# Kernel optimization log

Measured on AMD Instinct MI355X. Metric: run time of the kernel, lower is better.

The kernel has to match this reference:

```python
import jax, jax.numpy as jnp
import numpy as np

NEG_INF = -9e15  # matches torch's -9000000000000000.0 mask value
ALPHA = 0.2      # LeakyReLU negative slope


def setup_inputs() -> dict:
    key = jax.random.key(0)
    k1, k2, k3, k4 = jax.random.split(key, 4)
    B, N, Fin, Fout, H = 32, 512, 256, 64, 8
    x = jax.random.normal(k1, (B, N, Fin), dtype=jnp.float32)
    adj = (jax.random.uniform(k2, (B, N, N)) < 0.5).astype(jnp.float32)
    # W: Linear(in_features, out_features*n_heads, bias=False) weight, stored as (Fin, Fout*H)
    W = jax.random.normal(k3, (Fin, Fout * H), dtype=jnp.float32) / np.sqrt(Fin).astype(np.float32)
    # a: attention vector per head over concat(src,dst) features -> (H, 2*Fout)
    a = jax.random.normal(k4, (H, 2 * Fout), dtype=jnp.float32) * 0.1
    return {"x": x, "adj": adj, "W": W, "a": a}


def reference(x, adj, W, a):
    # x: (B,N,Fin), adj: (B,N,N), W: (Fin, H*F), a: (H, 2F)
    B, N, _ = x.shape
    H, twoF = a.shape
    F = twoF // 2
    h = (x @ W).reshape(B, N, H, F)  # (B,N,H,F)
    # Decompose concat-score: e_ij = lrelu(h_i . a_src + h_j . a_dst) -- same math
    # as (cat(h_i,h_j) * a).sum(-1) without materializing (B,N,N,H,2F).
    s_src = jnp.einsum('bnhf,hf->bnh', h, a[:, :F])  # (B,N,H)
    s_dst = jnp.einsum('bnhf,hf->bnh', h, a[:, F:])  # (B,N,H)
    e = s_src[:, :, None, :] + s_dst[:, None, :, :]  # (B,N,N,H)
    e = jax.nn.leaky_relu(e, negative_slope=ALPHA)
    e = jnp.where(adj[..., None] > 0, e, NEG_INF)
    attn = jax.nn.softmax(e, axis=2)  # softmax over neighbors j (dim=2)
    # dropout omitted (eval mode / p effectively 0 for the reference baseline)
    h_prime = jnp.einsum('bijh,bjhf->bihf', attn, h)  # (B,N,H,F)
    return h_prime.reshape(B, N, H * F)  # concat=True
```

## Files before the change

kernel.cpp:

```cpp
#include <hip/hip_runtime.h>
#include <hip/hip_bf16.h>
#include <stdint.h>


#define ALPHA  0.2f
#define ESCALE 1.4426950408889634f

typedef __bf16 bf16x8 __attribute__((ext_vector_type(8)));
typedef __bf16 bf16x4 __attribute__((ext_vector_type(4)));
typedef float  f32x4  __attribute__((ext_vector_type(4)));

#if __has_builtin(__builtin_amdgcn_exp2f)
#define EXP2(x) __builtin_amdgcn_exp2f(x)
#else
#define EXP2(x) exp2f(x)
#endif

#define HT_STRIDE 520
#define WT_STRIDE 264

__device__ inline bf16x8 ld8(const float* p) {
    float4 a0 = *(const float4*)p;
    float4 a1 = *(const float4*)(p + 4);
    bf16x8 r;
    r[0]=(__bf16)a0.x; r[1]=(__bf16)a0.y; r[2]=(__bf16)a0.z; r[3]=(__bf16)a0.w;
    r[4]=(__bf16)a1.x; r[5]=(__bf16)a1.y; r[6]=(__bf16)a1.z; r[7]=(__bf16)a1.w;
    return r;
}

__global__ __launch_bounds__(512) void k0_all(const float* __restrict__ x,
                                              const float* __restrict__ W,
                                              const float* __restrict__ adj,
                                              __bf16* __restrict__ xbf,
                                              __bf16* __restrict__ Wbf,
                                              unsigned* __restrict__ mask) {
    __shared__ float tile[64][65];
    const int blk = blockIdx.x, tid = threadIdx.x;
    if (blk < 1024) {
        long c = (long)blk * 512 + tid;
        int s  = (int)(c & 7);
        int r  = (int)((c >> 3) & 511);
        int kc = (int)((c >> 12) & 3);
        int b  = (int)(c >> 14);
        const float* src = x + (((long)b * 512 + r) * 256 + kc * 64 + s * 8);
        float4 a0 = *(const float4*)src;
        float4 a1 = *(const float4*)(src + 4);
        bf16x8 o;
        o[0]=(__bf16)a0.x; o[1]=(__bf16)a0.y; o[2]=(__bf16)a0.z; o[3]=(__bf16)a0.w;
        o[4]=(__bf16)a1.x; o[5]=(__bf16)a1.y; o[6]=(__bf16)a1.z; o[7]=(__bf16)a1.w;
        *(bf16x8*)(xbf + c * 8) = o;
    } else if (blk < 1056) {
        int bi = blk - 1024;
        int kt = bi & 3, ft = bi >> 2;
        int ff = tid & 63;
        #pragma unroll
        for (int i = 0; i < 8; ++i) {
            int kk = (tid >> 6) + i * 8;
            tile[kk][ff] = W[(long)(kt * 64 + kk) * 512 + ft * 64 + ff];
        }
        __syncthreads();
        int kk2 = tid & 63;
        #pragma unroll
        for (int i = 0; i < 8; ++i) {
            int ff2 = (tid >> 6) + i * 8;
            Wbf[(long)(ft * 64 + ff2) * 256 + kt * 64 + kk2] = (__bf16)tile[kk2][ff2];
        }
    } else {
        const int T2 = (blk - 1056) * 512 + tid;
        const int w    = T2 & 3;
        const int quad = (T2 >> 2) & 3;
        const int row  = (T2 >> 4) & 511;
        const int b    = T2 >> 13;
        const float* p = adj + ((long)b * 512 + row) * 512 + quad * 8;
        unsigned word = 0;
        #pragma unroll
        for (int k = 0; k < 4; ++k) {
            const float* qp = p + (w * 4 + k) * 32;
            float4 a0 = *(const float4*)qp;
            float4 a1 = *(const float4*)(qp + 4);
            unsigned byte =  (a0.x > 0.f ? 1u : 0u)
                          | ((a0.y > 0.f ? 1u : 0u) << 1)
                          | ((a0.z > 0.f ? 1u : 0u) << 2)
                          | ((a0.w > 0.f ? 1u : 0u) << 3)
                          | ((a1.x > 0.f ? 1u : 0u) << 4)
                          | ((a1.y > 0.f ? 1u : 0u) << 5)
                          | ((a1.z > 0.f ? 1u : 0u) << 6)
                          | ((a1.w > 0.f ? 1u : 0u) << 7);
            word |= byte << (8 * k);
        }
        mask[T2] = word;
    }
}

struct SmemK1 {
    __bf16 Wt[64 * 256];
    __bf16 Xt[256 * 64];
    float  asrc[64], adst[64];
};

__global__ __launch_bounds__(512, 4) void k1_gemm(const __bf16* __restrict__ xbf,
                                                  const __bf16* __restrict__ Wbf,
                                                  const float* __restrict__ a,
                                                  __bf16* __restrict__ hT,
                                                  float* __restrict__ ssrc,
                                                  float* __restrict__ sdst) {
    __shared__ SmemK1 sm;
    const int b = blockIdx.x, h = blockIdx.y, zz = blockIdx.z;
    const int tid  = threadIdx.x;
    const int wave = tid >> 6, lane = tid & 63;
    const int quad = lane >> 4, col = lane & 15;
    const int row0 = zz * 256;

    if (tid < 128) {
        float v = a[h * 128 + tid] * ESCALE;
        if (tid < 64) sm.asrc[tid] = v; else sm.adst[tid - 64] = v;
    }
    {
        const uint4* src = (const uint4*)(Wbf + (long)h * 64 * 256);
        #pragma unroll
        for (int i = 0; i < 4; ++i) {
            int c = tid + i * 512;
            int f = c >> 5, s = c & 31;
            int sw = (s & 24) | ((s & 7) ^ (f & 7));
            *(uint4*)((char*)sm.Wt + f * 512 + sw * 16) = src[c];
        }
    }
    {
        const uint4* src = (const uint4*)(xbf + (((long)b * 4 + 0) * 512 + row0) * 64);
        #pragma unroll
        for (int i = 0; i < 4; ++i) {
            int c = tid + i * 512;
            int r = c >> 3, s = c & 7;
            *(uint4*)((char*)sm.Xt + r * 128 + ((s ^ (r & 7)) * 16)) = src[c];
        }
    }
    __syncthreads();

    f32x4 acc[2][4] = {};
    #pragma unroll
    for (int kc = 0; kc < 4; ++kc) {
        #pragma unroll
        for (int sk = 0; sk < 2; ++sk) {
            bf16x8 av[2], bv[4];
            #pragma unroll
            for (int it = 0; it < 2; ++it) {
                int r = wave * 32 + it * 16 + col;
                int g = (sk * 4 + quad) ^ (r & 7);
                av[it] = *(const bf16x8*)((const char*)sm.Xt + r * 128 + g * 16);
            }
            #pragma unroll
            for (int nt = 0; nt < 4; ++nt) {
                int n = nt * 16 + col;
                int G = kc * 8 + sk * 4 + quad;
                int Gs = (G & 24) | ((G & 7) ^ (n & 7));
                bv[nt] = *(const bf16x8*)((const char*)sm.Wt + n * 512 + Gs * 16);
            }
            #pragma unroll
            for (int it = 0; it < 2; ++it)
                #pragma unroll
                for (int nt = 0; nt < 4; ++nt)
                    acc[it][nt] = __builtin_amdgcn_mfma_f32_16x16x32_bf16(av[it], bv[nt], acc[it][nt], 0, 0, 0);
        }
        if (kc < 3) {
            __syncthreads();
            const uint4* src = (const uint4*)(xbf + (((long)b * 4 + kc + 1) * 512 + row0) * 64);
            #pragma unroll
            for (int i = 0; i < 4; ++i) {
                int c = tid + i * 512;
                int r = c >> 3, s = c & 7;
                *(uint4*)((char*)sm.Xt + r * 128 + ((s ^ (r & 7)) * 16)) = src[c];
            }
            __syncthreads();
        }
    }

    const long bh = (long)b * 8 + h;
    {
        #pragma unroll
        for (int it = 0; it < 2; ++it)
            #pragma unroll
            for (int nt = 0; nt < 4; ++nt) {
                int f = nt * 16 + col;
                int j = row0 + wave * 32 + it * 16 + quad * 4;
                bf16x4 pk = { (__bf16)acc[it][nt][0], (__bf16)acc[it][nt][1],
                              (__bf16)acc[it][nt][2], (__bf16)acc[it][nt][3] };
                *(bf16x4*)(hT + (bh * 64 + f) * HT_STRIDE + j) = pk;
            }
    }
    {
        float asr[4], adr[4];
        #pragma unroll
        for (int nt = 0; nt < 4; ++nt) {
            asr[nt] = sm.asrc[nt * 16 + col];
            adr[nt] = sm.adst[nt * 16 + col];
        }
        #pragma unroll
        for (int it = 0; it < 2; ++it)
            #pragma unroll
            for (int r = 0; r < 4; ++r) {
                float ps = 0.f, pd = 0.f;
                #pragma unroll
                for (int nt = 0; nt < 4; ++nt) {
                    ps += acc[it][nt][r] * asr[nt];
                    pd += acc[it][nt][r] * adr[nt];
                }
                #pragma unroll
                for (int m = 1; m <= 8; m <<= 1) {
                    ps += __shfl_xor(ps, m, 64);
                    pd += __shfl_xor(pd, m, 64);
                }
                if (col == 0) {
                    int j = row0 + wave * 32 + it * 16 + quad * 4 + r;
                    ssrc[bh * 512 + j] = ps;
                    sdst[bh * 512 + j] = pd;
                }
            }
    }
}

struct SmemK2 {
    __bf16 hT[64][HT_STRIDE];
    float  sds[512];
};

__global__ __launch_bounds__(512, 4) void k2_attn(const uint4* __restrict__ mask,
                                                  const __bf16* __restrict__ hT,
                                                  const float* __restrict__ ssrc,
                                                  const float* __restrict__ sdst,
                                                  float* __restrict__ out) {
    __shared__ SmemK2 sm;
    const int b = blockIdx.x, h = blockIdx.y, q = blockIdx.z;
    const int tid  = threadIdx.x;
    const int wave = tid >> 6, lane = tid & 63;
    const int quad = lane >> 4, col = lane & 15;
    const long bh = (long)b * 8 + h;
    const int rowbase = q * 256 + wave * 32;

    {
        const uint4* src = (const uint4*)(hT + bh * 64 * HT_STRIDE);
        uint4* dst = (uint4*)&sm.hT[0][0];
        #pragma unroll
        for (int t = 0; t < 8; ++t)
            dst[t * 512 + tid] = src[t * 512 + tid];
        if (tid < 64) dst[4096 + tid] = src[4096 + tid];
    }
    sm.sds[tid] = sdst[bh * 512 + tid];

    float si[2]; uint4 mk[2];
    #pragma unroll
    for (int it = 0; it < 2; ++it) {
        int i = rowbase + it * 16 + col;
        si[it] = ssrc[bh * 512 + i];
        mk[it] = mask[((long)b * 512 + i) * 4 + quad];
    }
    __syncthreads();

    bf16x8 ones;
    #pragma unroll
    for (int u = 0; u < 8; ++u) ones[u] = (__bf16)1.0f;

    f32x4 acc[2][4] = {};
    f32x4 accs[2]   = {};

    #pragma unroll
    for (int ks = 0; ks < 16; ++ks) {
        const int j0 = ks * 32 + quad * 8;
        f32x4 s0 = *(const f32x4*)&sm.sds[j0];
        f32x4 s1 = *(const f32x4*)&sm.sds[j0 + 4];
        float sd[8] = {s0[0],s0[1],s0[2],s0[3],s1[0],s1[1],s1[2],s1[3]};
        unsigned mb[2];
        #pragma unroll
        for (int it = 0; it < 2; ++it) {
            unsigned wrd = (ks < 4) ? mk[it].x : (ks < 8) ? mk[it].y
                         : (ks < 12) ? mk[it].z : mk[it].w;
            mb[it] = (wrd >> ((ks & 3) * 8)) & 0xFFu;
        }
        bf16x8 P[2];
        #pragma unroll
        for (int it = 0; it < 2; ++it)
            #pragma unroll
            for (int u = 0; u < 8; ++u) {
                float e = si[it] + sd[u];
                float l = fmaxf(e, ALPHA * e);
                float xv = EXP2(l);
                P[it][u] = (__bf16)(((mb[it] >> u) & 1u) ? xv : 0.0f);
            }
        bf16x8 bv[4];
        #pragma unroll
        for (int nt = 0; nt < 4; ++nt)
            bv[nt] = *(const bf16x8*)(&sm.hT[nt * 16 + col][j0]);
        #pragma unroll
        for (int it = 0; it < 2; ++it) {
            #pragma unroll
            for (int nt = 0; nt < 4; ++nt)
                acc[it][nt] = __builtin_amdgcn_mfma_f32_16x16x32_bf16(P[it], bv[nt], acc[it][nt], 0, 0, 0);
            accs[it] = __builtin_amdgcn_mfma_f32_16x16x32_bf16(P[it], ones, accs[it], 0, 0, 0);
        }
    }
    #pragma unroll
    for (int it = 0; it < 2; ++it)
        #pragma unroll
        for (int r = 0; r < 4; ++r) {
            float s = accs[it][r];
            float inv = (s > 0.f) ? 1.0f / s : 0.f;
            int i = rowbase + it * 16 + quad * 4 + r;
            float* orow = out + ((long)b * 512 + i) * 512 + h * 64;
            #pragma unroll
            for (int nt = 0; nt < 4; ++nt)
                orow[nt * 16 + col] = acc[it][nt][r] * inv;
        }
}

struct SmemF {
    __bf16 hT[64][HT_STRIDE];
    __bf16 WT[64][WT_STRIDE];
    float  ssrc[512], sdst[512];
    float  asrc[64], adst[64];
};

__global__ __launch_bounds__(1024, 4) void k_gat_fused(const float* __restrict__ x,
                                                       const float* __restrict__ adj,
                                                       const float* __restrict__ W,
                                                       const float* __restrict__ a,
                                                       float* __restrict__ out) {
    __shared__ SmemF sm;
    const int b = blockIdx.x, h = blockIdx.y;
    const int tid  = threadIdx.x;
    const int wave = tid >> 6, lane = tid & 63;
    const int quad = lane >> 4, col = lane & 15;

    if (tid < 128) {
        float v = a[h * 128 + tid] * ESCALE;
        if (tid < 64) sm.asrc[tid] = v; else sm.adst[tid - 64] = v;
    }
    {
        int c = tid & 63, k0 = tid >> 6;
        #pragma unroll 4
        for (int t = 0; t < 16; ++t)
            sm.WT[c][k0 + t * 16] = (__bf16)W[(long)(k0 + t * 16) * 512 + h * 64 + c];
    }
    __syncthreads();
    {
        const float* xb = x + (long)b * 512 * 256;
        f32x4 acc[2][4] = {};
        for (int ks = 0; ks < 8; ++ks) {
            int k0 = ks * 32 + quad * 8;
            bf16x8 av[2], bv[4];
            #pragma unroll
            for (int it = 0; it < 2; ++it)
                av[it] = ld8(xb + (long)(wave * 32 + it * 16 + col) * 256 + k0);
            #pragma unroll
            for (int nt = 0; nt < 4; ++nt)
                bv[nt] = *(const bf16x8*)(&sm.WT[nt * 16 + col][k0]);
            #pragma unroll
            for (int it = 0; it < 2; ++it)
                #pragma unroll
                for (int nt = 0; nt < 4; ++nt)
                    acc[it][nt] = __builtin_amdgcn_mfma_f32_16x16x32_bf16(av[it], bv[nt], acc[it][nt], 0, 0, 0);
        }
        #pragma unroll
        for (int it = 0; it < 2; ++it)
            #pragma unroll
            for (int nt = 0; nt < 4; ++nt) {
                int f = nt * 16 + col;
                int j = wave * 32 + it * 16 + quad * 4;
                bf16x4 pk = { (__bf16)acc[it][nt][0], (__bf16)acc[it][nt][1],
                              (__bf16)acc[it][nt][2], (__bf16)acc[it][nt][3] };
                *(bf16x4*)(&sm.hT[f][j]) = pk;
            }
    }
    __syncthreads();
    {
        int j = tid & 511;
        float s = 0.f;
        if (tid < 512) {
            #pragma unroll 8
            for (int f = 0; f < 64; ++f) s += (float)sm.hT[f][j] * sm.asrc[f];
            sm.ssrc[j] = s;
        } else {
            #pragma unroll 8
            for (int f = 0; f < 64; ++f) s += (float)sm.hT[f][j] * sm.adst[f];
            sm.sdst[j] = s;
        }
    }
    __syncthreads();
    {
        float si[2];
        const float* arow[2];
        #pragma unroll
        for (int it = 0; it < 2; ++it) {
            int i = wave * 32 + it * 16 + col;
            si[it]   = sm.ssrc[i];
            arow[it] = adj + ((long)b * 512 + i) * 512;
        }
        bf16x8 ones;
        #pragma unroll
        for (int u = 0; u < 8; ++u) ones[u] = (__bf16)1.0f;
        f32x4 acc[2][4] = {};
        f32x4 accs[2]   = {};
        float4 pa0[2], pa1[2];
        #pragma unroll
        for (int it = 0; it < 2; ++it) {
            pa0[it] = *(const float4*)(arow[it] + quad * 8);
            pa1[it] = *(const float4*)(arow[it] + quad * 8 + 4);
        }
        for (int ks = 0; ks < 16; ++ks) {
            int j0 = ks * 32 + quad * 8;
            f32x4 s0 = *(const f32x4*)&sm.sdst[j0];
            f32x4 s1 = *(const f32x4*)&sm.sdst[j0 + 4];
            float sd[8] = {s0[0],s0[1],s0[2],s0[3],s1[0],s1[1],s1[2],s1[3]};
            float am[2][8];
            #pragma unroll
            for (int it = 0; it < 2; ++it) {
                am[it][0]=pa0[it].x; am[it][1]=pa0[it].y;
                am[it][2]=pa0[it].z; am[it][3]=pa0[it].w;
                am[it][4]=pa1[it].x; am[it][5]=pa1[it].y;
                am[it][6]=pa1[it].z; am[it][7]=pa1[it].w;
            }
            if (ks < 15) {
                #pragma unroll
                for (int it = 0; it < 2; ++it) {
                    pa0[it] = *(const float4*)(arow[it] + j0 + 32);
                    pa1[it] = *(const float4*)(arow[it] + j0 + 36);
                }
            }
            bf16x8 P[2];
            #pragma unroll
            for (int it = 0; it < 2; ++it)
                #pragma unroll
                for (int u = 0; u < 8; ++u) {
                    float e = si[it] + sd[u];
                    float l = fmaxf(e, ALPHA * e);
                    float p = am[it][u] * EXP2(l);
                    P[it][u] = (__bf16)p;
                }
            bf16x8 bv[4];
            #pragma unroll
            for (int nt = 0; nt < 4; ++nt)
                bv[nt] = *(const bf16x8*)(&sm.hT[nt * 16 + col][j0]);
            #pragma unroll
            for (int it = 0; it < 2; ++it) {
                #pragma unroll
                for (int nt = 0; nt < 4; ++nt)
                    acc[it][nt] = __builtin_amdgcn_mfma_f32_16x16x32_bf16(P[it], bv[nt], acc[it][nt], 0, 0, 0);
                accs[it] = __builtin_amdgcn_mfma_f32_16x16x32_bf16(P[it], ones, accs[it], 0, 0, 0);
            }
        }
        #pragma unroll
        for (int it = 0; it < 2; ++it)
            #pragma unroll
            for (int r = 0; r < 4; ++r) {
                float s = accs[it][r];
                float inv = (s > 0.f) ? 1.0f / s : 0.f;
                int i = wave * 32 + it * 16 + quad * 4 + r;
                float* orow = out + ((long)b * 512 + i) * 512 + h * 64;
                #pragma unroll
                for (int nt = 0; nt < 4; ++nt)
                    orow[nt * 16 + col] = acc[it][nt][r] * inv;
            }
    }
}

extern "C" void kernel_launch(void* const* d_in, const int* in_sizes, int n_in,
                              void* d_out, int out_size, void* d_ws, size_t ws_size,
                              hipStream_t stream) {
    const float* x   = (const float*)d_in[0];
    const float* adj = (const float*)d_in[1];
    const float* W   = (const float*)d_in[2];
    const float* a   = (const float*)d_in[3];
    float* out = (float*)d_out;

    const size_t HT_BYTES   = 256ull * 64 * HT_STRIDE * 2;
    const size_t SC_BYTES   = 32ull * 8 * 512 * 4;
    const size_t MASK_BYTES = 32ull * 512 * 64;
    const size_t XBF_BYTES  = 32ull * 512 * 256 * 2;
    const size_t WBF_BYTES  = 512ull * 256 * 2;
    const size_t NEED = HT_BYTES + 2 * SC_BYTES + MASK_BYTES
                      + XBF_BYTES + WBF_BYTES;

    if (d_ws && ws_size >= NEED) {
        char* p = (char*)d_ws;
        __bf16* hT   = (__bf16*)p;                 p += HT_BYTES;
        float* ssrc  = (float*)p;                  p += SC_BYTES;
        float* sdst  = (float*)p;                  p += SC_BYTES;
        unsigned* mk = (unsigned*)p;               p += MASK_BYTES;
        __bf16* xbf  = (__bf16*)p;                 p += XBF_BYTES;
        __bf16* Wbf  = (__bf16*)p;
        k0_all<<<1568, 512, 0, stream>>>(x, W, adj, xbf, Wbf, mk);
        k1_gemm<<<dim3(32, 8, 2), 512, 0, stream>>>(xbf, Wbf, a, hT, ssrc, sdst);
        k2_attn<<<dim3(32, 8, 2), 512, 0, stream>>>((const uint4*)mk, hT, ssrc, sdst, out);
    } else {
        k_gat_fused<<<dim3(32, 8), 1024, 0, stream>>>(x, adj, W, a, out);
    }
}
```

Baseline: 148.1 us.

## Split hT into two halves and overlap second-half load with first-half compute

The k1 output layout for hT becomes two 256-column halves with padded row stride. k2_attn copies the first half into shared memory, keeps the second half's global loads in registers while computing over the first 8 k-steps, then stores them and syncs before the remaining steps. The score computation is also rewritten using paired float2 vector ops. This aims to hide the global load latency of the prologue, at the cost of more registers, which could reduce occupancy under the 4-block launch bound.

```diff
diff --git a/kernel.cpp b/kernel.cpp
--- a/kernel.cpp
+++ b/kernel.cpp
@@ -9,6 +9,7 @@
 typedef __bf16 bf16x8 __attribute__((ext_vector_type(8)));
 typedef __bf16 bf16x4 __attribute__((ext_vector_type(4)));
 typedef float  f32x4  __attribute__((ext_vector_type(4)));
+typedef float  f32x2  __attribute__((ext_vector_type(2)));
 
 #if __has_builtin(__builtin_amdgcn_exp2f)
 #define EXP2(x) __builtin_amdgcn_exp2f(x)
@@ -18,6 +19,7 @@
 
 #define HT_STRIDE 520
 #define WT_STRIDE 264
+#define HROW 264
 
 __device__ inline bf16x8 ld8(const float* p) {
     float4 a0 = *(const float4*)p;
@@ -175,6 +177,7 @@
     }
 
     const long bh = (long)b * 8 + h;
+    __bf16* hTb = hT + bh * (2 * 64 * HROW);
     {
         #pragma unroll
         for (int it = 0; it < 2; ++it)
@@ -182,9 +185,10 @@
             for (int nt = 0; nt < 4; ++nt) {
                 int f = nt * 16 + col;
                 int j = row0 + wave * 32 + it * 16 + quad * 4;
+                int half = j >> 8, jj = j & 255;
                 bf16x4 pk = { (__bf16)acc[it][nt][0], (__bf16)acc[it][nt][1],
                               (__bf16)acc[it][nt][2], (__bf16)acc[it][nt][3] };
-                *(bf16x4*)(hT + (bh * 64 + f) * HT_STRIDE + j) = pk;
+                *(bf16x4*)(hTb + (half * 64 + f) * HROW + jj) = pk;
             }
     }
     {
@@ -219,9 +223,52 @@
 }
 
 struct SmemK2 {
-    __bf16 hT[64][HT_STRIDE];
+    __bf16 hTh[2][64][HROW];
     float  sds[512];
 };
+
+#define K2STEP(KS, HF)                                                         \
+    {                                                                          \
+        const int j0  = (KS) * 32 + quad * 8;        \
+        const int jj0 = ((KS) & 7) * 32 + quad * 8;       \
+        f32x4 s0 = *(const f32x4*)&sm.sds[j0];                                 \
+        f32x4 s1 = *(const f32x4*)&sm.sds[j0 + 4];                             \
+        f32x2 sp[4] = { {s0[0],s0[1]}, {s0[2],s0[3]},                          \
+                        {s1[0],s1[1]}, {s1[2],s1[3]} };                        \
+        unsigned mb[2];                                                        \
+        _Pragma("unroll")                                                      \
+        for (int it = 0; it < 2; ++it) {                                       \
+            unsigned wrd = ((KS) < 4) ? mk[it].x : ((KS) < 8) ? mk[it].y       \
+                         : ((KS) < 12) ? mk[it].z : mk[it].w;                  \
+            mb[it] = (wrd >> (((KS) & 3) * 8)) & 0xFFu;                        \
+        }                                                                      \
+        bf16x8 P[2];                                                           \
+        _Pragma("unroll")                                                      \
+        for (int it = 0; it < 2; ++it) {                                       \
+            f32x2 siv = { si[it], si[it] };                                    \
+            _Pragma("unroll")                                                  \
+            for (int p = 0; p < 4; ++p) {                  \
+                f32x2 e  = sp[p] + siv;                      \
+                f32x2 ea = e * ALPHA;                        \
+                float l0 = fmaxf(e[0], ea[0]);                                 \
+                float l1 = fmaxf(e[1], ea[1]);                                 \
+                float x0 = EXP2(l0), x1 = EXP2(l1);                            \
+                P[it][2*p]   = (__bf16)(((mb[it] >> (2*p))   & 1u) ? x0 : 0.f);\
+                P[it][2*p+1] = (__bf16)(((mb[it] >> (2*p+1)) & 1u) ? x1 : 0.f);\
+            }                                                                  \
+        }                                                                      \
+        bf16x8 bv[4];                                                          \
+        _Pragma("unroll")                                                      \
+        for (int nt = 0; nt < 4; ++nt)                                         \
+            bv[nt] = *(const bf16x8*)(&sm.hTh[HF][nt * 16 + col][jj0]);        \
+        _Pragma("unroll")                                                      \
+        for (int it = 0; it < 2; ++it) {                                       \
+            _Pragma("unroll")                                                  \
+            for (int nt = 0; nt < 4; ++nt)                                     \
+                acc[it][nt] = __builtin_amdgcn_mfma_f32_16x16x32_bf16(P[it], bv[nt], acc[it][nt], 0, 0, 0); \
+            accs[it] = __builtin_amdgcn_mfma_f32_16x16x32_bf16(P[it], ones, accs[it], 0, 0, 0); \
+        }                                                                      \
+    }
 
 __global__ __launch_bounds__(512, 4) void k2_attn(const uint4* __restrict__ mask,
                                                   const __bf16* __restrict__ hT,
@@ -236,13 +283,20 @@
     const long bh = (long)b * 8 + h;
     const int rowbase = q * 256 + wave * 32;
 
-    {
-        const uint4* src = (const uint4*)(hT + bh * 64 * HT_STRIDE);
-        uint4* dst = (uint4*)&sm.hT[0][0];
-        #pragma unroll
-        for (int t = 0; t < 8; ++t)
-            dst[t * 512 + tid] = src[t * 512 + tid];
-        if (tid < 64) dst[4096 + tid] = src[4096 + tid];
+    const __bf16* hTb = hT + bh * (2 * 64 * HROW);
+    const uint4* srcH0 = (const uint4*)hTb;
+    const uint4* srcH1 = (const uint4*)(hTb + 64 * HROW);
+
+    uint4 h1[4]; uint4 h1x = {};
+    #pragma unroll
+    for (int i = 0; i < 4; ++i) h1[i] = srcH1[tid + i * 512];
+    if (tid < 64) h1x = srcH1[2048 + tid];
+
+    {
+        uint4* dst = (uint4*)&sm.hTh[0][0][0];
+        #pragma unroll
+        for (int i = 0; i < 4; ++i) dst[tid + i * 512] = srcH0[tid + i * 512];
+        if (tid < 64) dst[2048 + tid] = srcH0[2048 + tid];
     }
     sm.sds[tid] = sdst[bh * 512 + tid];
 
@@ -263,40 +317,21 @@
     f32x4 accs[2]   = {};
 
     #pragma unroll
-    for (int ks = 0; ks < 16; ++ks) {
-        const int j0 = ks * 32 + quad * 8;
-        f32x4 s0 = *(const f32x4*)&sm.sds[j0];
-        f32x4 s1 = *(const f32x4*)&sm.sds[j0 + 4];
-        float sd[8] = {s0[0],s0[1],s0[2],s0[3],s1[0],s1[1],s1[2],s1[3]};
-        unsigned mb[2];
-        #pragma unroll
-        for (int it = 0; it < 2; ++it) {
-            unsigned wrd = (ks < 4) ? mk[it].x : (ks < 8) ? mk[it].y
-                         : (ks < 12) ? mk[it].z : mk[it].w;
-            mb[it] = (wrd >> ((ks & 3) * 8)) & 0xFFu;
-        }
-        bf16x8 P[2];
-        #pragma unroll
-        for (int it = 0; it < 2; ++it)
-            #pragma unroll
-            for (int u = 0; u < 8; ++u) {
-                float e = si[it] + sd[u];
-                float l = fmaxf(e, ALPHA * e);
-                float xv = EXP2(l);
-                P[it][u] = (__bf16)(((mb[it] >> u) & 1u) ? xv : 0.0f);
-            }
-        bf16x8 bv[4];
-        #pragma unroll
-        for (int nt = 0; nt < 4; ++nt)
-            bv[nt] = *(const bf16x8*)(&sm.hT[nt * 16 + col][j0]);
-        #pragma unroll
-        for (int it = 0; it < 2; ++it) {
-            #pragma unroll
-            for (int nt = 0; nt < 4; ++nt)
-                acc[it][nt] = __builtin_amdgcn_mfma_f32_16x16x32_bf16(P[it], bv[nt], acc[it][nt], 0, 0, 0);
-            accs[it] = __builtin_amdgcn_mfma_f32_16x16x32_bf16(P[it], ones, accs[it], 0, 0, 0);
-        }
-    }
+    for (int ks = 0; ks < 8; ++ks)
+        K2STEP(ks, 0)
+
+    {
+        uint4* dst = (uint4*)&sm.hTh[1][0][0];
+        #pragma unroll
+        for (int i = 0; i < 4; ++i) dst[tid + i * 512] = h1[i];
+        if (tid < 64) dst[2048 + tid] = h1x;
+    }
+    __syncthreads();
+
+    #pragma unroll
+    for (int ks = 8; ks < 16; ++ks)
+        K2STEP(ks, 1)
+
     #pragma unroll
     for (int it = 0; it < 2; ++it)
         #pragma unroll
@@ -470,7 +505,7 @@
     const float* a   = (const float*)d_in[3];
     float* out = (float*)d_out;
 
-    const size_t HT_BYTES   = 256ull * 64 * HT_STRIDE * 2;
+    const size_t HT_BYTES   = 256ull * 2 * 64 * HROW * 2;
     const size_t SC_BYTES   = 32ull * 8 * 512 * 4;
     const size_t MASK_BYTES = 32ull * 512 * 64;
     const size_t XBF_BYTES  = 32ull * 512 * 256 * 2;
```

Result: no change. 148.5 us (+0.2%).

## Split attention hT into two halves to halve LDS and double k2 blocks

Applied to the files above, without the earlier changes.

The hT workspace is re-laid out as two 256-column halves per (batch, head). k2_attn now loads one half into shared memory at a time, synchronising between halves, so it uses about half the LDS. The kernel also handles 16 rows per wave instead of 32, is launched with twice as many blocks, and raises the occupancy hint to 8 blocks per CU. The aim is more concurrent waves and better latency hiding. The cost is an extra barrier and reload per block, and each hT tile is now read by twice as many blocks, with less MFMA work per wave.

```diff
diff --git a/kernel.cpp b/kernel.cpp
--- a/kernel.cpp
+++ b/kernel.cpp
@@ -18,6 +18,7 @@
 
 #define HT_STRIDE 520
 #define WT_STRIDE 264
+#define HROW 264
 
 __device__ inline bf16x8 ld8(const float* p) {
     float4 a0 = *(const float4*)p;
@@ -175,6 +176,7 @@
     }
 
     const long bh = (long)b * 8 + h;
+    __bf16* hTb = hT + bh * (2 * 64 * HROW);
     {
         #pragma unroll
         for (int it = 0; it < 2; ++it)
@@ -182,9 +184,10 @@
             for (int nt = 0; nt < 4; ++nt) {
                 int f = nt * 16 + col;
                 int j = row0 + wave * 32 + it * 16 + quad * 4;
+                int half = j >> 8, jj = j & 255;
                 bf16x4 pk = { (__bf16)acc[it][nt][0], (__bf16)acc[it][nt][1],
                               (__bf16)acc[it][nt][2], (__bf16)acc[it][nt][3] };
-                *(bf16x4*)(hT + (bh * 64 + f) * HT_STRIDE + j) = pk;
+                *(bf16x4*)(hTb + (half * 64 + f) * HROW + jj) = pk;
             }
     }
     {
@@ -219,11 +222,11 @@
 }
 
 struct SmemK2 {
-    __bf16 hT[64][HT_STRIDE];
+    __bf16 hTh[64][HROW];
     float  sds[512];
 };
 
-__global__ __launch_bounds__(512, 4) void k2_attn(const uint4* __restrict__ mask,
+__global__ __launch_bounds__(512, 8) void k2_attn(const uint4* __restrict__ mask,
                                                   const __bf16* __restrict__ hT,
                                                   const float* __restrict__ ssrc,
                                                   const float* __restrict__ sdst,
@@ -234,81 +237,105 @@
     const int wave = tid >> 6, lane = tid & 63;
     const int quad = lane >> 4, col = lane & 15;
     const long bh = (long)b * 8 + h;
-    const int rowbase = q * 256 + wave * 32;
-
-    {
-        const uint4* src = (const uint4*)(hT + bh * 64 * HT_STRIDE);
-        uint4* dst = (uint4*)&sm.hT[0][0];
-        #pragma unroll
-        for (int t = 0; t < 8; ++t)
-            dst[t * 512 + tid] = src[t * 512 + tid];
-        if (tid < 64) dst[4096 + tid] = src[4096 + tid];
+    const int rowbase = q * 128 + wave * 16;
+
+    const __bf16* hTb = hT + bh * (2 * 64 * HROW);
+    const uint4* srcH0 = (const uint4*)hTb;
+    const uint4* srcH1 = (const uint4*)(hTb + 64 * HROW);
+
+    {
+        uint4* dst = (uint4*)&sm.hTh[0][0];
+        #pragma unroll
+        for (int i = 0; i < 4; ++i) dst[tid + i * 512] = srcH0[tid + i * 512];
+        if (tid < 64) dst[2048 + tid] = srcH0[2048 + tid];
     }
     sm.sds[tid] = sdst[bh * 512 + tid];
 
-    float si[2]; uint4 mk[2];
-    #pragma unroll
-    for (int it = 0; it < 2; ++it) {
-        int i = rowbase + it * 16 + col;
-        si[it] = ssrc[bh * 512 + i];
-        mk[it] = mask[((long)b * 512 + i) * 4 + quad];
-    }
+    const int i0 = rowbase + col;
+    const float si = ssrc[bh * 512 + i0];
+    const uint4 mk = mask[((long)b * 512 + i0) * 4 + quad];
     __syncthreads();
 
     bf16x8 ones;
     #pragma unroll
     for (int u = 0; u < 8; ++u) ones[u] = (__bf16)1.0f;
 
-    f32x4 acc[2][4] = {};
-    f32x4 accs[2]   = {};
+    f32x4 acc[4] = {};
+    f32x4 accs   = {};
 
     #pragma unroll
-    for (int ks = 0; ks < 16; ++ks) {
-        const int j0 = ks * 32 + quad * 8;
+    for (int ks = 0; ks < 8; ++ks) {
+        const int j0  = ks * 32 + quad * 8;
+        const int jj0 = j0;
         f32x4 s0 = *(const f32x4*)&sm.sds[j0];
         f32x4 s1 = *(const f32x4*)&sm.sds[j0 + 4];
         float sd[8] = {s0[0],s0[1],s0[2],s0[3],s1[0],s1[1],s1[2],s1[3]};
-        unsigned mb[2];
-        #pragma unroll
-        for (int it = 0; it < 2; ++it) {
-            unsigned wrd = (ks < 4) ? mk[it].x : (ks < 8) ? mk[it].y
-                         : (ks < 12) ? mk[it].z : mk[it].w;
-            mb[it] = (wrd >> ((ks & 3) * 8)) & 0xFFu;
-        }
-        bf16x8 P[2];
-        #pragma unroll
-        for (int it = 0; it < 2; ++it)
-            #pragma unroll
-            for (int u = 0; u < 8; ++u) {
-                float e = si[it] + sd[u];
-                float l = fmaxf(e, ALPHA * e);
-                float xv = EXP2(l);
-                P[it][u] = (__bf16)(((mb[it] >> u) & 1u) ? xv : 0.0f);
-            }
+        unsigned wrd = (ks < 4) ? mk.x : mk.y;
+        unsigned mb  = (wrd >> ((ks & 3) * 8)) & 0xFFu;
+        bf16x8 P;
+        #pragma unroll
+        for (int u = 0; u < 8; ++u) {
+            float e = si + sd[u];
+            float l = fmaxf(e, ALPHA * e);
+            float xv = EXP2(l);
+            P[u] = (__bf16)(((mb >> u) & 1u) ? xv : 0.0f);
+        }
         bf16x8 bv[4];
         #pragma unroll
         for (int nt = 0; nt < 4; ++nt)
-            bv[nt] = *(const bf16x8*)(&sm.hT[nt * 16 + col][j0]);
-        #pragma unroll
-        for (int it = 0; it < 2; ++it) {
-            #pragma unroll
-            for (int nt = 0; nt < 4; ++nt)
-                acc[it][nt] = __builtin_amdgcn_mfma_f32_16x16x32_bf16(P[it], bv[nt], acc[it][nt], 0, 0, 0);
-            accs[it] = __builtin_amdgcn_mfma_f32_16x16x32_bf16(P[it], ones, accs[it], 0, 0, 0);
-        }
-    }
+            bv[nt] = *(const bf16x8*)(&sm.hTh[nt * 16 + col][jj0]);
+        #pragma unroll
+        for (int nt = 0; nt < 4; ++nt)
+            acc[nt] = __builtin_amdgcn_mfma_f32_16x16x32_bf16(P, bv[nt], acc[nt], 0, 0, 0);
+        accs = __builtin_amdgcn_mfma_f32_16x16x32_bf16(P, ones, accs, 0, 0, 0);
+    }
+
+    __syncthreads();
+    {
+        uint4* dst = (uint4*)&sm.hTh[0][0];
+        #pragma unroll
+        for (int i = 0; i < 4; ++i) dst[tid + i * 512] = srcH1[tid + i * 512];
+        if (tid < 64) dst[2048 + tid] = srcH1[2048 + tid];
+    }
+    __syncthreads();
+
     #pragma unroll
-    for (int it = 0; it < 2; ++it)
-        #pragma unroll
-        for (int r = 0; r < 4; ++r) {
-            float s = accs[it][r];
-            float inv = (s > 0.f) ? 1.0f / s : 0.f;
-            int i = rowbase + it * 16 + quad * 4 + r;
-            float* orow = out + ((long)b * 512 + i) * 512 + h * 64;
-            #pragma unroll
-            for (int nt = 0; nt < 4; ++nt)
-                orow[nt * 16 + col] = acc[it][nt][r] * inv;
-        }
+    for (int ks = 8; ks < 16; ++ks) {
+        const int j0  = ks * 32 + quad * 8;
+        const int jj0 = (ks - 8) * 32 + quad * 8;
+        f32x4 s0 = *(const f32x4*)&sm.sds[j0];
+        f32x4 s1 = *(const f32x4*)&sm.sds[j0 + 4];
+        float sd[8] = {s0[0],s0[1],s0[2],s0[3],s1[0],s1[1],s1[2],s1[3]};
+        unsigned wrd = (ks < 12) ? mk.z : mk.w;
+        unsigned mb  = (wrd >> ((ks & 3) * 8)) & 0xFFu;
+        bf16x8 P;
+        #pragma unroll
+        for (int u = 0; u < 8; ++u) {
+            float e = si + sd[u];
+            float l = fmaxf(e, ALPHA * e);
+            float xv = EXP2(l);
+            P[u] = (__bf16)(((mb >> u) & 1u) ? xv : 0.0f);
+        }
+        bf16x8 bv[4];
+        #pragma unroll
+        for (int nt = 0; nt < 4; ++nt)
+            bv[nt] = *(const bf16x8*)(&sm.hTh[nt * 16 + col][jj0]);
+        #pragma unroll
+        for (int nt = 0; nt < 4; ++nt)
+            acc[nt] = __builtin_amdgcn_mfma_f32_16x16x32_bf16(P, bv[nt], acc[nt], 0, 0, 0);
+        accs = __builtin_amdgcn_mfma_f32_16x16x32_bf16(P, ones, accs, 0, 0, 0);
+    }
+
+    #pragma unroll
+    for (int r = 0; r < 4; ++r) {
+        float s = accs[r];
+        float inv = (s > 0.f) ? 1.0f / s : 0.f;
+        int i = rowbase + quad * 4 + r;
+        float* orow = out + ((long)b * 512 + i) * 512 + h * 64;
+        #pragma unroll
+        for (int nt = 0; nt < 4; ++nt)
+            orow[nt * 16 + col] = acc[nt][r] * inv;
+    }
 }
 
 struct SmemF {
@@ -470,7 +497,7 @@
     const float* a   = (const float*)d_in[3];
     float* out = (float*)d_out;
 
-    const size_t HT_BYTES   = 256ull * 64 * HT_STRIDE * 2;
+    const size_t HT_BYTES   = 256ull * 2 * 64 * HROW * 2;
     const size_t SC_BYTES   = 32ull * 8 * 512 * 4;
     const size_t MASK_BYTES = 32ull * 512 * 64;
     const size_t XBF_BYTES  = 32ull * 512 * 256 * 2;
@@ -488,7 +515,7 @@
         __bf16* Wbf  = (__bf16*)p;
         k0_all<<<1568, 512, 0, stream>>>(x, W, adj, xbf, Wbf, mk);
         k1_gemm<<<dim3(32, 8, 2), 512, 0, stream>>>(xbf, Wbf, a, hT, ssrc, sdst);
-        k2_attn<<<dim3(32, 8, 2), 512, 0, stream>>>((const uint4*)mk, hT, ssrc, sdst, out);
+        k2_attn<<<dim3(32, 8, 4), 512, 0, stream>>>((const uint4*)mk, hT, ssrc, sdst, out);
     } else {
         k_gat_fused<<<dim3(32, 8), 1024, 0, stream>>>(x, adj, W, a, out);
     }
```

New measurement: 157.7 us. +6.4%, slower.
